# Kernel optimization log

Hardware: AMD Instinct MI355X
Metric: run time of the kernel (lower is better)

## Reference

```python
import math
import jax, jax.numpy as jnp
import numpy as np

D_MODEL = 768
N_HEADS = 12
HEAD_DIM = D_MODEL // N_HEADS
D_FF = 3072
LN_EPS = 1e-5


def _alibi_slopes(n_heads):
    def pow2(n):
        start = 2 ** (-(2 ** (-(math.log2(n) - 3))))
        return [start * start ** i for i in range(n)]
    if n_heads & (n_heads - 1) == 0:
        s = pow2(n_heads)
    else:
        c = 2 ** math.floor(math.log2(n_heads))
        s = pow2(c) + pow2(2 * c)[0::2][: n_heads - c]
    return np.asarray(s, dtype=np.float32)  # positive; negated at use site


def _ln(t, g, b):
    m = jnp.mean(t, axis=-1, keepdims=True)
    v = jnp.mean(jnp.square(t - m), axis=-1, keepdims=True)
    return (t - m) * jax.lax.rsqrt(v + LN_EPS) * g + b


def setup_inputs() -> dict:
    key = jax.random.key(0)
    ks = jax.random.split(key, 12)
    B, N = 4, 1025
    s = 0.02
    inp = {
        "x": jax.random.normal(ks[0], (B, N, D_MODEL), dtype=jnp.float32),
        "positions": jax.random.normal(ks[1], (B, N, 2), dtype=jnp.float32) * 8.0,
        "patch_sizes": jax.random.uniform(ks[2], (B,), dtype=jnp.float32, minval=0.5, maxval=2.0),
        "num_registers": 0,
        "ln1_g": jnp.ones((D_MODEL,), jnp.float32),
        "ln1_b": jnp.zeros((D_MODEL,), jnp.float32),
        "wq": jax.random.normal(ks[3], (D_MODEL, D_MODEL), jnp.float32) * s,
        "bq": jnp.zeros((D_MODEL,), jnp.float32),
        "wk": jax.random.normal(ks[4], (D_MODEL, D_MODEL), jnp.float32) * s,
        "bk": jnp.zeros((D_MODEL,), jnp.float32),
        "wv": jax.random.normal(ks[5], (D_MODEL, D_MODEL), jnp.float32) * s,
        "bv": jnp.zeros((D_MODEL,), jnp.float32),
        "wo": jax.random.normal(ks[6], (D_MODEL, D_MODEL), jnp.float32) * s,
        "bo": jnp.zeros((D_MODEL,), jnp.float32),
        "qn_g": jnp.ones((HEAD_DIM,), jnp.float32),
        "qn_b": jnp.zeros((HEAD_DIM,), jnp.float32),
        "kn_g": jnp.ones((HEAD_DIM,), jnp.float32),
        "kn_b": jnp.zeros((HEAD_DIM,), jnp.float32),
        "ln2_g": jnp.ones((D_MODEL,), jnp.float32),
        "ln2_b": jnp.zeros((D_MODEL,), jnp.float32),
        "w1": jax.random.normal(ks[7], (D_MODEL, D_FF), jnp.float32) * s,
        "b1": jnp.zeros((D_FF,), jnp.float32),
        "w2": jax.random.normal(ks[8], (D_FF, D_MODEL), jnp.float32) * s,
        "b2": jnp.zeros((D_MODEL,), jnp.float32),
    }
    return inp


def reference(x, positions, patch_sizes, num_registers,
              ln1_g, ln1_b, wq, bq, wk, bk, wv, bv, wo, bo,
              qn_g, qn_b, kn_g, kn_b, ln2_g, ln2_b, w1, b1, w2, b2):
    B, N, d = x.shape
    H, HD = N_HEADS, HEAD_DIM

    xn = _ln(x, ln1_g, ln1_b)
    q = (xn @ wq + bq).reshape(B, N, H, HD).transpose(0, 2, 1, 3)  # [B,H,N,HD]
    k = (xn @ wk + bk).reshape(B, N, H, HD).transpose(0, 2, 1, 3)
    v = (xn @ wv + bv).reshape(B, N, H, HD).transpose(0, 2, 1, 3)
    q = _ln(q, qn_g, qn_b)  # qk-norm over head_dim
    k = _ln(k, kn_g, kn_b)

    # 2-D ALiBi bias: [B,H,N,N]
    slopes = jnp.asarray(_alibi_slopes(H))  # positive
    ps = jnp.clip(patch_sizes, 1e-6)[:, None, None]
    diff = positions[:, :, None, :] - positions[:, None, :, :]  # [B,N,N,2]
    dist = jnp.sqrt(jnp.sum(jnp.square(diff), axis=-1)) / ps  # [B,N,N]
    bias = -slopes[None, :, None, None] * dist[:, None, :, :]
    idx = jnp.arange(N)
    special = (idx == 0) | ((idx >= 1) & (idx < 1 + num_registers))  # CLS + registers
    keep = (~special).astype(x.dtype)
    bias = bias * keep[None, None, :, None] * keep[None, None, None, :]

    scale = 1.0 / math.sqrt(HD)
    scores = jnp.einsum('bhqd,bhkd->bhqk', q, k) * scale + bias
    attn = jax.nn.softmax(scores, axis=-1)
    o = jnp.einsum('bhqk,bhkd->bhqd', attn, v)
    o = o.transpose(0, 2, 1, 3).reshape(B, N, d) @ wo + bo
    x = x + o

    xn2 = _ln(x, ln2_g, ln2_b)
    mlp = jax.nn.gelu(xn2 @ w1 + b1, approximate=False) @ w2 + b2
    return x + mlp
```

## Files before the change

kernel.cpp:

```cpp
#include <hip/hip_runtime.h>
#include <hip/hip_bf16.h>
#include <math.h>

typedef __attribute__((ext_vector_type(4))) float f32x4;
typedef __attribute__((ext_vector_type(8))) short short8;

#define DMODEL 768
#define NH 12
#define HD 64
#define DFF 3072
#define KVB 64
#define NSPLIT 3
#define QH 2
#define NP 1040

struct FalseC { static constexpr bool v = false; };
struct TrueC  { static constexpr bool v = true;  };

__device__ __forceinline__ short f2bf(float f) {
    union { float f; unsigned int u; } c; c.f = f;
    unsigned int r = c.u + 0x7FFFu + ((c.u >> 16) & 1u);
    return (short)(r >> 16);
}

__device__ __forceinline__ float bf2f(short s) {
    union { unsigned int u; float f; } c; c.u = ((unsigned int)(unsigned short)s) << 16;
    return c.f;
}

__device__ __forceinline__ void gload16(const void* g, void* l) {
    __builtin_amdgcn_global_load_lds((const __attribute__((address_space(1))) void*)g,
                                     (__attribute__((address_space(3))) void*)l, 16, 0, 0);
}

__device__ __forceinline__ int xcd_swz(int o, int nwg) {
    int q = nwg >> 3, r = nwg & 7, x = o & 7, i = o >> 3;
    return (x < r ? x * (q + 1) : r * (q + 1) + (x - r) * q) + i;
}

__global__ __launch_bounds__(256) void transpose_cast(const float* __restrict__ src,
                                                      short* __restrict__ dst, int K, int Nn) {
    __shared__ float tile[32][33];
    const int n0 = blockIdx.x * 32, k0 = blockIdx.y * 32;
    const int tx = threadIdx.x & 31, ty = threadIdx.x >> 5;
    #pragma unroll
    for (int i = ty; i < 32; i += 8) {
        int k = k0 + i, n = n0 + tx;
        tile[i][tx] = (k < K && n < Nn) ? src[(size_t)k * Nn + n] : 0.f;
    }
    __syncthreads();
    #pragma unroll
    for (int i = ty; i < 32; i += 8) {
        int n = n0 + i, k = k0 + tx;
        if (n < Nn && k < K) dst[(size_t)n * K + k] = f2bf(tile[tx][i]);
    }
}

__global__ void concat_bias(const float* __restrict__ bq, const float* __restrict__ bk,
                            const float* __restrict__ bv, float* __restrict__ out) {
    int i = blockIdx.x * 256 + threadIdx.x;
    if (i < 2304) out[i] = (i < 768) ? bq[i] : (i < 1536 ? bk[i - 768] : bv[i - 1536]);
}

__global__ __launch_bounds__(256) void ln_rows(const float* __restrict__ x, const float* __restrict__ g,
                                               const float* __restrict__ bb, short* __restrict__ out, int M) {
    __shared__ float red[8];
    const int row = blockIdx.x;
    const int tid = threadIdx.x;
    const float* xr = x + (size_t)row * DMODEL;
    float v[3];
    #pragma unroll
    for (int j = 0; j < 3; j++) v[j] = xr[tid + j * 256];
    float s = v[0] + v[1] + v[2];
    #pragma unroll
    for (int mk = 32; mk; mk >>= 1) s += __shfl_xor(s, mk);
    if ((tid & 63) == 0) red[tid >> 6] = s;
    __syncthreads();
    const float mean = (red[0] + red[1] + red[2] + red[3]) * (1.0f / 768.0f);
    float sq = 0.f;
    #pragma unroll
    for (int j = 0; j < 3; j++) { float d = v[j] - mean; sq += d * d; }
    #pragma unroll
    for (int mk = 32; mk; mk >>= 1) sq += __shfl_xor(sq, mk);
    if ((tid & 63) == 0) red[4 + (tid >> 6)] = sq;
    __syncthreads();
    const float var = (red[4] + red[5] + red[6] + red[7]) * (1.0f / 768.0f);
    const float rstd = rsqrtf(var + 1e-5f);
    short* orow = out + (size_t)row * DMODEL;
    #pragma unroll
    for (int j = 0; j < 3; j++) {
        int col = tid + j * 256;
        orow[col] = f2bf((v[j] - mean) * rstd * g[col] + bb[col]);
    }
}

__global__ __launch_bounds__(256) void gemm_qkv(const short* __restrict__ A, const short* __restrict__ Bt,
        const float* __restrict__ bias,
        const float* __restrict__ qg, const float* __restrict__ qb2,
        const float* __restrict__ kg, const float* __restrict__ kb2,
        short* __restrict__ Qb, short* __restrict__ Kb, short* __restrict__ Vtp,
        int M, int B, int Nseq) {
    __shared__ short As[64 * 64];
    __shared__ short Bs[128 * 64];
    const int nbx = 18, nby = (M + 63) / 64;
    const int sid = xcd_swz(blockIdx.x, nbx * nby);
    const int n0 = (sid % nbx) * 128, m0 = (sid / nbx) * 64;
    const int tid = threadIdx.x, w = tid >> 6, lane = tid & 63, g = lane >> 4, cl = lane & 15;
    const int wm = w >> 1, wn = w & 1;
    f32x4 acc[2][4];
    #pragma unroll
    for (int a = 0; a < 2; a++)
        #pragma unroll
        for (int b2 = 0; b2 < 4; b2++) acc[a][b2] = (f32x4){0.f, 0.f, 0.f, 0.f};
    for (int kk = 0; kk < 768; kk += 64) {
        #pragma unroll
        for (int c = 0; c < 1536; c += 256) {
            int ci = c + tid;
            if (ci < 512) {
                int row = ci >> 3, p = ci & 7;
                int arow = m0 + row; if (arow >= M) arow = M - 1;
                gload16(A + (size_t)arow * 768 + kk + ((p ^ (row & 7)) << 3), &As[ci * 8]);
            } else {
                int c2 = ci - 512;
                int row = c2 >> 3, p = c2 & 7;
                gload16(Bt + (size_t)(n0 + row) * 768 + kk + ((p ^ (row & 7)) << 3), &Bs[c2 * 8]);
            }
        }
        __syncthreads();
        #pragma unroll
        for (int kh = 0; kh < 2; ++kh) {
            short8 af[2], bf[4];
            #pragma unroll
            for (int mi = 0; mi < 2; mi++) {
                int ra = wm * 32 + mi * 16 + cl;
                af[mi] = *(const short8*)&As[ra * 64 + ((((kh << 2) + g) ^ (ra & 7)) << 3)];
            }
            #pragma unroll
            for (int ni = 0; ni < 4; ni++) {
                int rb = wn * 64 + ni * 16 + cl;
                bf[ni] = *(const short8*)&Bs[rb * 64 + ((((kh << 2) + g) ^ (rb & 7)) << 3)];
            }
            #pragma unroll
            for (int mi = 0; mi < 2; mi++)
                #pragma unroll
                for (int ni = 0; ni < 4; ni++)
                    acc[mi][ni] = __builtin_amdgcn_mfma_f32_16x16x32_bf16(af[mi], bf[ni], acc[mi][ni], 0, 0, 0);
        }
        __syncthreads();
    }
    const int t = n0 / 768;
    const int h = (n0 - t * 768) / 64 + wn;
    const int b0 = m0 / Nseq, bnd = (b0 + 1) * Nseq;
    float bi[4];
    #pragma unroll
    for (int ni = 0; ni < 4; ni++) bi[ni] = bias[n0 + wn * 64 + ni * 16 + cl];
    if (t < 2) {
        const float* gp = (t == 0) ? qg : kg;
        const float* bp = (t == 0) ? qb2 : kb2;
        float gv[4], bv[4];
        #pragma unroll
        for (int ni = 0; ni < 4; ni++) { gv[ni] = gp[ni * 16 + cl]; bv[ni] = bp[ni * 16 + cl]; }
        short* out = (t == 0) ? Qb : Kb;
        #pragma unroll
        for (int mi = 0; mi < 2; mi++)
            #pragma unroll
            for (int r = 0; r < 4; r++) {
                int row = m0 + wm * 32 + mi * 16 + 4 * g + r;
                float v0 = acc[mi][0][r] + bi[0];
                float v1 = acc[mi][1][r] + bi[1];
                float v2 = acc[mi][2][r] + bi[2];
                float v3 = acc[mi][3][r] + bi[3];
                float sx = v0 + v1 + v2 + v3;
                float sxx = v0 * v0 + v1 * v1 + v2 * v2 + v3 * v3;
                #pragma unroll
                for (int mk = 8; mk; mk >>= 1) { sx += __shfl_xor(sx, mk); sxx += __shfl_xor(sxx, mk); }
                float mean = sx * (1.0f / 64.0f);
                float var = sxx * (1.0f / 64.0f) - mean * mean;
                float rstd = rsqrtf(var + 1e-5f);
                if (row < M) {
                    int bb = (row >= bnd) ? b0 + 1 : b0;
                    int n = row - bb * Nseq;
                    size_t base = (((size_t)bb * NH + h) * Nseq + n) * HD + cl;
                    out[base + 0]  = f2bf(fmaf((v0 - mean) * rstd, gv[0], bv[0]));
                    out[base + 16] = f2bf(fmaf((v1 - mean) * rstd, gv[1], bv[1]));
                    out[base + 32] = f2bf(fmaf((v2 - mean) * rstd, gv[2], bv[2]));
                    out[base + 48] = f2bf(fmaf((v3 - mean) * rstd, gv[3], bv[3]));
                }
            }
    } else {
        #pragma unroll
        for (int mi = 0; mi < 2; mi++)
            #pragma unroll
            for (int r = 0; r < 4; r++) {
                int row = m0 + wm * 32 + mi * 16 + 4 * g + r;
                if (row < M) {
                    int bb = (row >= bnd) ? b0 + 1 : b0;
                    int n = row - bb * Nseq;
                    size_t vb2 = ((size_t)bb * NH + h) * HD + cl;
                    #pragma unroll
                    for (int ni = 0; ni < 4; ni++)
                        Vtp[(vb2 + ni * 16) * NP + n] = f2bf(acc[mi][ni][r] + bi[ni]);
                }
            }
    }
}

template<int EPI, int BM, int BN>
__global__ __launch_bounds__(256) void gemm_bt(const short* __restrict__ A, const short* __restrict__ Bt,
        const float* __restrict__ bias, const float* __restrict__ res, void* __restrict__ Cv,
        int M, int Nn, int K) {
    constexpr int RM = BM / 32, RN = BN / 32;
    __shared__ short As[BM * 64];
    __shared__ short Bs[BN * 64];
    const int nbx = Nn / BN, nby = (M + BM - 1) / BM;
    const int sid = xcd_swz(blockIdx.x, nbx * nby);
    const int n0 = (sid % nbx) * BN, m0 = (sid / nbx) * BM;
    const int tid = threadIdx.x, w = tid >> 6, lane = tid & 63, g = lane >> 4, cl = lane & 15;
    const int wm = w >> 1, wn = w & 1;
    f32x4 acc[RM][RN];
    #pragma unroll
    for (int a = 0; a < RM; a++)
        #pragma unroll
        for (int b2 = 0; b2 < RN; b2++) acc[a][b2] = (f32x4){0.f, 0.f, 0.f, 0.f};
    constexpr int CHA = BM * 8, CHT = (BM + BN) * 8;
    for (int kk = 0; kk < K; kk += 64) {
        #pragma unroll
        for (int c = 0; c < CHT; c += 256) {
            int ci = c + tid;
            if (ci < CHA) {
                int row = ci >> 3, p = ci & 7;
                int arow = m0 + row; if (arow >= M) arow = M - 1;
                gload16(A + (size_t)arow * K + kk + ((p ^ (row & 7)) << 3), &As[ci * 8]);
            } else {
                int c2 = ci - CHA;
                int row = c2 >> 3, p = c2 & 7;
                gload16(Bt + (size_t)(n0 + row) * K + kk + ((p ^ (row & 7)) << 3), &Bs[c2 * 8]);
            }
        }
        __syncthreads();
        #pragma unroll
        for (int kh = 0; kh < 2; ++kh) {
            short8 af[RM], bf[RN];
            #pragma unroll
            for (int mi = 0; mi < RM; mi++) {
                int ra = wm * (BM / 2) + mi * 16 + cl;
                af[mi] = *(const short8*)&As[ra * 64 + ((((kh << 2) + g) ^ (ra & 7)) << 3)];
            }
            #pragma unroll
            for (int ni = 0; ni < RN; ni++) {
                int rb = wn * (BN / 2) + ni * 16 + cl;
                bf[ni] = *(const short8*)&Bs[rb * 64 + ((((kh << 2) + g) ^ (rb & 7)) << 3)];
            }
            #pragma unroll
            for (int mi = 0; mi < RM; mi++)
                #pragma unroll
                for (int ni = 0; ni < RN; ni++)
                    acc[mi][ni] = __builtin_amdgcn_mfma_f32_16x16x32_bf16(af[mi], bf[ni], acc[mi][ni], 0, 0, 0);
        }
        __syncthreads();
    }
    #pragma unroll
    for (int ni = 0; ni < RN; ++ni) {
        int col = n0 + wn * (BN / 2) + ni * 16 + cl;
        float bi = bias[col];
        #pragma unroll
        for (int mi = 0; mi < RM; ++mi) {
            int rb = m0 + wm * (BM / 2) + mi * 16 + 4 * g;
            #pragma unroll
            for (int r = 0; r < 4; ++r) {
                int row = rb + r;
                if (row < M) {
                    float vv = acc[mi][ni][r] + bi;
                    if (EPI == 1) {
                        vv += res[(size_t)row * Nn + col];
                        ((float*)Cv)[(size_t)row * Nn + col] = vv;
                    } else {
                        float ge = 0.5f * vv * (1.0f + erff(vv * 0.70710678118654752f));
                        ((short*)Cv)[(size_t)row * Nn + col] = f2bf(ge);
                    }
                }
            }
        }
    }
}

__global__ __launch_bounds__(256, 3) void attn_kernel(
        const short* __restrict__ Qb, const short* __restrict__ Kb, const short* __restrict__ Vt,
        const float* __restrict__ pos, const float* __restrict__ psz, const int* __restrict__ nregp,
        short* __restrict__ opart, float* __restrict__ ppart, int B, int Nn, int nwg) {
    __shared__ short Vbuf[2][QH][4096];
    __shared__ short Pl[4][QH][16][68];
    __shared__ float Rs[4][QH][16];
    const int nqt = (Nn + 63) >> 6;
    const int sid = xcd_swz(blockIdx.x, nwg);
    const int qt = sid % nqt;
    const int rem = sid / nqt;
    const int nyy = (NH / QH) * NSPLIT;
    const int yy = rem % nyy;
    const int b = rem / nyy;
    const int h0 = (yy / NSPLIT) * QH, sp = yy % NSPLIT;
    const int tid = threadIdx.x, w = tid >> 6, lane = tid & 63, g = lane >> 4, cl = lane & 15;
    const int nreg1 = 1 + nregp[0];
    const float inv_ps = 1.0f / fmaxf(psz[b], 1e-6f);
    const float sc2 = 0.125f * 1.4426950408889634f;
    const size_t bq = (size_t)b * Nn;
    const float2* __restrict__ pos2 = (const float2*)pos;
    const int q0 = qt * 64 + w * 16;

    size_t bh[QH], vb[QH];
    short8 qa[QH][2];
    float sP[QH];
    int qr = q0 + cl; if (qr > Nn - 1) qr = Nn - 1;
    const float2 qp = pos2[bq + qr];
    const float keepq = (qr < nreg1) ? 0.f : 1.f;
    #pragma unroll
    for (int hh = 0; hh < QH; hh++) {
        int h = h0 + hh;
        bh[hh] = ((size_t)b * NH + h) * (size_t)Nn;
        vb[hh] = ((size_t)b * NH + h) * (size_t)(HD * NP);
        float slope = (h < 8) ? exp2f(-(float)(h + 1)) : exp2f(-0.5f - (float)(h - 8));
        sP[hh] = slope * inv_ps * 1.4426950408889634f * keepq;
        const short* qptr = Qb + (bh[hh] + qr) * HD;
        qa[hh][0] = *(const short8*)(qptr + 8 * g);
        qa[hh][1] = *(const short8*)(qptr + 32 + 8 * g);
    }

    int qi[4];
    #pragma unroll
    for (int i = 0; i < 4; i++) qi[i] = q0 + 4 * g + i;

    f32x4 o[QH][4];
    float psum[QH] = {0.f, 0.f};
    #pragma unroll
    for (int hh = 0; hh < QH; hh++)
        #pragma unroll
        for (int c2 = 0; c2 < 4; c2++) o[hh][c2] = (f32x4){0.f, 0.f, 0.f, 0.f};

    const int ktiles = (Nn + KVB - 1) / KVB;
    const int tps = (ktiles + NSPLIT - 1) / NSPLIT;
    const int t0 = sp * tps, t1 = min(ktiles, t0 + tps);

    auto stage = [&](int buf, int kt) {
        const int kv0 = kt * KVB;
        #pragma unroll
        for (int it = 0; it < 2 * QH; ++it) {
            int idx = it * 256 + tid;
            int hh = idx >> 9, rm = idx & 511;
            int d = rm >> 3, slot = rm & 7;
            int kvs = kv0 + ((slot ^ (d & 7)) << 3);
            gload16(Vt + vb[hh] + (size_t)d * NP + kvs, &Vbuf[buf][hh][rm * 8]);
        }
    };

    stage(0, t0);
    int cur = 0;
    for (int kt = t0; kt < t1; ++kt) {
        const int kv0 = kt * KVB;
        __syncthreads();
        if (kt + 1 < t1) stage(cur ^ 1, kt + 1);

        auto qbody = [&](int qt2, auto mc, auto tc) {
            constexpr bool KMASK = decltype(mc)::v;
            constexpr bool TAIL  = decltype(tc)::v;
            const int kbase = kv0 + qt2 * 16;
            int krow = kbase + cl;
            if (TAIL) krow = min(krow, Nn - 1);
            const short* kp0 = Kb + (bh[0] + krow) * HD;
            const short* kp1 = Kb + (bh[1] + krow) * HD;
            const short8 k00 = *(const short8*)(kp0 + 8 * g);
            const short8 k01 = *(const short8*)(kp0 + 32 + 8 * g);
            const short8 k10 = *(const short8*)(kp1 + 8 * g);
            const short8 k11 = *(const short8*)(kp1 + 32 + 8 * g);
            f32x4 s0 = __builtin_amdgcn_mfma_f32_16x16x32_bf16(k00, qa[0][0], (f32x4){0.f,0.f,0.f,0.f}, 0, 0, 0);
            s0 = __builtin_amdgcn_mfma_f32_16x16x32_bf16(k01, qa[0][1], s0, 0, 0, 0);
            f32x4 s1 = __builtin_amdgcn_mfma_f32_16x16x32_bf16(k10, qa[1][0], (f32x4){0.f,0.f,0.f,0.f}, 0, 0, 0);
            s1 = __builtin_amdgcn_mfma_f32_16x16x32_bf16(k11, qa[1][1], s1, 0, 0, 0);
            const int kb4 = kbase + 4 * g;
            float p0v[4], p1v[4];
            #pragma unroll
            for (int i = 0; i < 4; i++) {
                int ki = kb4 + i;
                int kic = TAIL ? min(ki, Nn - 1) : ki;
                float2 kp2 = pos2[bq + kic];
                float dx = qp.x - kp2.x, dy = qp.y - kp2.y;
                float dist = sqrtf(fmaf(dx, dx, dy * dy));
                if (KMASK) dist *= (ki < nreg1) ? 0.f : 1.f;
                float e0 = fmaf(s0[i], sc2, -12.0f);
                e0 = fmaf(-sP[0], dist, e0);
                float p0 = exp2f(e0);
                float e1 = fmaf(s1[i], sc2, -12.0f);
                e1 = fmaf(-sP[1], dist, e1);
                float p1 = exp2f(e1);
                if (TAIL) { bool vl = ki < Nn; p0 = vl ? p0 : 0.f; p1 = vl ? p1 : 0.f; }
                psum[0] += p0; psum[1] += p1;
                p0v[i] = p0; p1v[i] = p1;
            }
            unsigned int w00, w01, w10, w11;
            asm("v_cvt_pk_bf16_f32 %0, %1, %2" : "=v"(w00) : "v"(p0v[0]), "v"(p0v[1]));
            asm("v_cvt_pk_bf16_f32 %0, %1, %2" : "=v"(w01) : "v"(p0v[2]), "v"(p0v[3]));
            asm("v_cvt_pk_bf16_f32 %0, %1, %2" : "=v"(w10) : "v"(p1v[0]), "v"(p1v[1]));
            asm("v_cvt_pk_bf16_f32 %0, %1, %2" : "=v"(w11) : "v"(p1v[2]), "v"(p1v[3]));
            *(unsigned int*)&Pl[w][0][cl][qt2 * 16 + 4 * g]     = w00;
            *(unsigned int*)&Pl[w][0][cl][qt2 * 16 + 4 * g + 2] = w01;
            *(unsigned int*)&Pl[w][1][cl][qt2 * 16 + 4 * g]     = w10;
            *(unsigned int*)&Pl[w][1][cl][qt2 * 16 + 4 * g + 2] = w11;
        };

        const bool istail = (kv0 + KVB > Nn);
        if (!istail) {
            if (kv0 < nreg1) {
                qbody(0, TrueC{}, FalseC{}); qbody(1, TrueC{}, FalseC{});
                qbody(2, TrueC{}, FalseC{}); qbody(3, TrueC{}, FalseC{});
            } else {
                qbody(0, FalseC{}, FalseC{}); qbody(1, FalseC{}, FalseC{});
                qbody(2, FalseC{}, FalseC{}); qbody(3, FalseC{}, FalseC{});
            }
        } else {
            qbody(0, FalseC{}, TrueC{}); qbody(1, FalseC{}, TrueC{});
            qbody(2, FalseC{}, TrueC{}); qbody(3, FalseC{}, TrueC{});
        }

        #pragma unroll
        for (int hh = 0; hh < QH; hh++) {
            #pragma unroll
            for (int ks = 0; ks < 2; ++ks) {
                const short8 pf = *(const short8*)&Pl[w][hh][cl][ks * 32 + 8 * g];
                #pragma unroll
                for (int c2 = 0; c2 < 4; c2++) {
                    const int d = c2 * 16 + cl;
                    const int slot = ((ks << 2) + g) ^ (cl & 7);
                    const short8 vf = *(const short8*)&Vbuf[cur][hh][d * 64 + slot * 8];
                    o[hh][c2] = __builtin_amdgcn_mfma_f32_16x16x32_bf16(pf, vf, o[hh][c2], 0, 0, 0);
                }
            }
        }
        cur ^= 1;
    }

    #pragma unroll
    for (int hh = 0; hh < QH; hh++) {
        float r = psum[hh];
        r += __shfl_xor(r, 16);
        r += __shfl_xor(r, 32);
        if (lane < 16) Rs[w][hh][lane] = r;
    }
    float4 rs0 = *(const float4*)&Rs[w][0][4 * g];
    float4 rs1 = *(const float4*)&Rs[w][1][4 * g];
    #pragma unroll
    for (int i = 0; i < 4; i++) {
        if (qi[i] < Nn) {
            #pragma unroll
            for (int hh = 0; hh < QH; hh++) {
                size_t rbase = (((size_t)sp * B + b) * NH + (h0 + hh)) * Nn + qi[i];
                #pragma unroll
                for (int c2 = 0; c2 < 4; c2++)
                    opart[rbase * HD + c2 * 16 + cl] = f2bf(o[hh][c2][i]);
                if (cl == 0) ppart[rbase] = hh ? rs1[i] : rs0[i];
            }
        }
    }
}

__global__ __launch_bounds__(256) void attn_reduce(const short* __restrict__ opart,
        const float* __restrict__ ppart, short* __restrict__ Ob, int B, int Nn) {
    const int rows = B * NH * Nn;
    const int row = blockIdx.x * 4 + (threadIdx.x >> 6);
    if (row >= rows) return;
    const int d = threadIdx.x & 63;
    const int n = row % Nn;
    const int bh = row / Nn;
    const int h = bh % NH, b = bh / NH;
    const size_t stride = (size_t)B * NH * Nn;
    float o = 0.f, p = 0.f;
    #pragma unroll
    for (int s = 0; s < NSPLIT; s++) {
        o += bf2f(opart[((size_t)s * stride + row) * HD + d]);
        p += ppart[(size_t)s * stride + row];
    }
    Ob[((size_t)b * Nn + n) * DMODEL + h * HD + d] = f2bf(o / p);
}

extern "C" void kernel_launch(void* const* d_in, const int* in_sizes, int n_in,
                              void* d_out, int out_size, void* d_ws, size_t ws_size,
                              hipStream_t stream) {
    const float* x    = (const float*)d_in[0];
    const float* pos  = (const float*)d_in[1];
    const float* psz  = (const float*)d_in[2];
    const int*   nreg = (const int*)d_in[3];
    const float* ln1g = (const float*)d_in[4];
    const float* ln1b = (const float*)d_in[5];
    const float* wq   = (const float*)d_in[6];
    const float* bq   = (const float*)d_in[7];
    const float* wk   = (const float*)d_in[8];
    const float* bk   = (const float*)d_in[9];
    const float* wv   = (const float*)d_in[10];
    const float* bv   = (const float*)d_in[11];
    const float* wo   = (const float*)d_in[12];
    const float* bo   = (const float*)d_in[13];
    const float* qng  = (const float*)d_in[14];
    const float* qnb  = (const float*)d_in[15];
    const float* kng  = (const float*)d_in[16];
    const float* knb  = (const float*)d_in[17];
    const float* ln2g = (const float*)d_in[18];
    const float* ln2b = (const float*)d_in[19];
    const float* w1   = (const float*)d_in[20];
    const float* b1   = (const float*)d_in[21];
    const float* w2   = (const float*)d_in[22];
    const float* b2   = (const float*)d_in[23];

    const int B  = in_sizes[2];
    const int Nn = in_sizes[1] / (2 * B);
    const int M  = B * Nn;

    char* ws = (char*)d_ws;
    size_t off = 0;
    auto alloc = [&](size_t bytes) -> char* {
        char* p = ws + off;
        off += (bytes + 255) & ~(size_t)255;
        return p;
    };
    short* wt_qkv   = (short*)alloc((size_t)2304 * 768 * 2);
    short* wt_o     = (short*)alloc((size_t)768 * 768 * 2);
    short* wt_1     = (short*)alloc((size_t)3072 * 768 * 2);
    short* wt_2     = (short*)alloc((size_t)768 * 3072 * 2);
    float* bias_qkv = (float*)alloc(2304 * 4);
    short* xn       = (short*)alloc((size_t)M * 768 * 2);
    short* Qb       = (short*)alloc((size_t)M * 768 * 2);
    short* Kb       = (short*)alloc((size_t)M * 768 * 2);
    short* Vt       = (short*)alloc((size_t)B * NH * HD * NP * 2 + 4096);
    short* Ob       = (short*)alloc((size_t)M * 768 * 2);
    float* x1       = (float*)alloc((size_t)M * 768 * 4);
    short* xn2      = (short*)alloc((size_t)M * 768 * 2);
    short* hmid     = (short*)alloc((size_t)M * 3072 * 2);
    float* ppart    = (float*)alloc((size_t)NSPLIT * B * NH * Nn * 4);
    short* opart    = hmid;

    dim3 blk(256);
    transpose_cast<<<dim3(24, 24), blk, 0, stream>>>(wq, wt_qkv, 768, 768);
    transpose_cast<<<dim3(24, 24), blk, 0, stream>>>(wk, wt_qkv + 768 * 768, 768, 768);
    transpose_cast<<<dim3(24, 24), blk, 0, stream>>>(wv, wt_qkv + 2 * 768 * 768, 768, 768);
    transpose_cast<<<dim3(24, 24), blk, 0, stream>>>(wo, wt_o, 768, 768);
    transpose_cast<<<dim3(96, 24), blk, 0, stream>>>(w1, wt_1, 768, 3072);
    transpose_cast<<<dim3(24, 96), blk, 0, stream>>>(w2, wt_2, 3072, 768);
    concat_bias<<<9, blk, 0, stream>>>(bq, bk, bv, bias_qkv);

    const int MB64 = (M + 63) / 64;
    const int MB128 = (M + 127) / 128;
    ln_rows<<<M, blk, 0, stream>>>(x, ln1g, ln1b, xn, M);
    gemm_qkv<<<18 * MB64, blk, 0, stream>>>(xn, wt_qkv, bias_qkv, qng, qnb, kng, knb,
                                            Qb, Kb, Vt, M, B, Nn);
    const int nqt = (Nn + 63) / 64;
    const int anwg = nqt * (NH / QH) * NSPLIT * B;
    attn_kernel<<<anwg, blk, 0, stream>>>(Qb, Kb, Vt, pos, psz, nreg, opart, ppart, B, Nn, anwg);
    attn_reduce<<<(B * NH * Nn + 3) / 4, blk, 0, stream>>>(opart, ppart, Ob, B, Nn);
    gemm_bt<1, 64, 64><<<12 * MB64, blk, 0, stream>>>(Ob, wt_o, bo, x, x1, M, 768, 768);
    ln_rows<<<M, blk, 0, stream>>>(x1, ln2g, ln2b, xn2, M);
    gemm_bt<2, 128, 128><<<24 * MB128, blk, 0, stream>>>(xn2, wt_1, b1, nullptr, hmid, M, 3072, 768);
    gemm_bt<1, 64, 64><<<12 * MB64, blk, 0, stream>>>(hmid, wt_2, b2, x1, (float*)d_out, M, 768, 3072);
}
```

Baseline: 283.1 us.

## Merge weight transposes, single-buffer attention V tile, retile FFN1 GEMM

```diff
diff --git a/kernel.cpp b/kernel.cpp
--- a/kernel.cpp
+++ b/kernel.cpp
@@ -38,10 +38,25 @@
     return (x < r ? x * (q + 1) : r * (q + 1) + (x - r) * q) + i;
 }
 
-__global__ __launch_bounds__(256) void transpose_cast(const float* __restrict__ src,
-                                                      short* __restrict__ dst, int K, int Nn) {
+__global__ __launch_bounds__(256) void transpose_all(
+        const float* __restrict__ wq, const float* __restrict__ wk, const float* __restrict__ wv,
+        const float* __restrict__ wo, const float* __restrict__ w1, const float* __restrict__ w2,
+        short* __restrict__ wt_qkv, short* __restrict__ wt_o,
+        short* __restrict__ wt_1, short* __restrict__ wt_2) {
     __shared__ float tile[32][33];
-    const int n0 = blockIdx.x * 32, k0 = blockIdx.y * 32;
+    int bid = blockIdx.x;
+    const float* src; short* dst; int K, Nn, nx;
+    if (bid < 2304) {
+        int s = bid / 576; bid -= s * 576;
+        src = (s == 0) ? wq : (s == 1) ? wk : (s == 2) ? wv : wo;
+        dst = (s < 3) ? (wt_qkv + (size_t)s * 768 * 768) : wt_o;
+        K = 768; Nn = 768; nx = 24;
+    } else if (bid < 4608) {
+        bid -= 2304; src = w1; dst = wt_1; K = 768; Nn = 3072; nx = 96;
+    } else {
+        bid -= 4608; src = w2; dst = wt_2; K = 3072; Nn = 768; nx = 24;
+    }
+    const int n0 = (bid % nx) * 32, k0 = (bid / nx) * 32;
     const int tx = threadIdx.x & 31, ty = threadIdx.x >> 5;
     #pragma unroll
     for (int i = ty; i < 32; i += 8) {
@@ -284,11 +299,11 @@
     }
 }
 
-__global__ __launch_bounds__(256, 3) void attn_kernel(
+__global__ __launch_bounds__(256, 4) void attn_kernel(
         const short* __restrict__ Qb, const short* __restrict__ Kb, const short* __restrict__ Vt,
         const float* __restrict__ pos, const float* __restrict__ psz, const int* __restrict__ nregp,
         short* __restrict__ opart, float* __restrict__ ppart, int B, int Nn, int nwg) {
-    __shared__ short Vbuf[2][QH][4096];
+    __shared__ short Vbuf[QH][4096];
     __shared__ short Pl[4][QH][16][68];
     __shared__ float Rs[4][QH][16];
     const int nqt = (Nn + 63) >> 6;
@@ -340,7 +355,7 @@
     const int tps = (ktiles + NSPLIT - 1) / NSPLIT;
     const int t0 = sp * tps, t1 = min(ktiles, t0 + tps);
 
-    auto stage = [&](int buf, int kt) {
+    auto stage = [&](int kt) {
         const int kv0 = kt * KVB;
         #pragma unroll
         for (int it = 0; it < 2 * QH; ++it) {
@@ -348,16 +363,13 @@
             int hh = idx >> 9, rm = idx & 511;
             int d = rm >> 3, slot = rm & 7;
             int kvs = kv0 + ((slot ^ (d & 7)) << 3);
-            gload16(Vt + vb[hh] + (size_t)d * NP + kvs, &Vbuf[buf][hh][rm * 8]);
+            gload16(Vt + vb[hh] + (size_t)d * NP + kvs, &Vbuf[hh][rm * 8]);
         }
     };
 
-    stage(0, t0);
-    int cur = 0;
+    stage(t0);
     for (int kt = t0; kt < t1; ++kt) {
         const int kv0 = kt * KVB;
-        __syncthreads();
-        if (kt + 1 < t1) stage(cur ^ 1, kt + 1);
 
         auto qbody = [&](int qt2, auto mc, auto tc) {
             constexpr bool KMASK = decltype(mc)::v;
@@ -420,6 +432,8 @@
             qbody(2, FalseC{}, TrueC{}); qbody(3, FalseC{}, TrueC{});
         }
 
+        __syncthreads();
+
         #pragma unroll
         for (int hh = 0; hh < QH; hh++) {
             #pragma unroll
@@ -429,12 +443,14 @@
                 for (int c2 = 0; c2 < 4; c2++) {
                     const int d = c2 * 16 + cl;
                     const int slot = ((ks << 2) + g) ^ (cl & 7);
-                    const short8 vf = *(const short8*)&Vbuf[cur][hh][d * 64 + slot * 8];
+                    const short8 vf = *(const short8*)&Vbuf[hh][d * 64 + slot * 8];
                     o[hh][c2] = __builtin_amdgcn_mfma_f32_16x16x32_bf16(pf, vf, o[hh][c2], 0, 0, 0);
                 }
             }
         }
-        cur ^= 1;
+
+        __syncthreads();
+        if (kt + 1 < t1) stage(kt + 1);
     }
 
     #pragma unroll
@@ -536,16 +552,10 @@
     short* opart    = hmid;
 
     dim3 blk(256);
-    transpose_cast<<<dim3(24, 24), blk, 0, stream>>>(wq, wt_qkv, 768, 768);
-    transpose_cast<<<dim3(24, 24), blk, 0, stream>>>(wk, wt_qkv + 768 * 768, 768, 768);
-    transpose_cast<<<dim3(24, 24), blk, 0, stream>>>(wv, wt_qkv + 2 * 768 * 768, 768, 768);
-    transpose_cast<<<dim3(24, 24), blk, 0, stream>>>(wo, wt_o, 768, 768);
-    transpose_cast<<<dim3(96, 24), blk, 0, stream>>>(w1, wt_1, 768, 3072);
-    transpose_cast<<<dim3(24, 96), blk, 0, stream>>>(w2, wt_2, 3072, 768);
+    transpose_all<<<6912, blk, 0, stream>>>(wq, wk, wv, wo, w1, w2, wt_qkv, wt_o, wt_1, wt_2);
     concat_bias<<<9, blk, 0, stream>>>(bq, bk, bv, bias_qkv);
 
     const int MB64 = (M + 63) / 64;
-    const int MB128 = (M + 127) / 128;
     ln_rows<<<M, blk, 0, stream>>>(x, ln1g, ln1b, xn, M);
     gemm_qkv<<<18 * MB64, blk, 0, stream>>>(xn, wt_qkv, bias_qkv, qng, qnb, kng, knb,
                                             Qb, Kb, Vt, M, B, Nn);
@@ -555,6 +565,6 @@
     attn_reduce<<<(B * NH * Nn + 3) / 4, blk, 0, stream>>>(opart, ppart, Ob, B, Nn);
     gemm_bt<1, 64, 64><<<12 * MB64, blk, 0, stream>>>(Ob, wt_o, bo, x, x1, M, 768, 768);
     ln_rows<<<M, blk, 0, stream>>>(x1, ln2g, ln2b, xn2, M);
-    gemm_bt<2, 128, 128><<<24 * MB128, blk, 0, stream>>>(xn2, wt_1, b1, nullptr, hmid, M, 3072, 768);
+    gemm_bt<2, 64, 128><<<24 * MB64, blk, 0, stream>>>(xn2, wt_1, b1, nullptr, hmid, M, 3072, 768);
     gemm_bt<1, 64, 64><<<12 * MB64, blk, 0, stream>>>(hmid, wt_2, b2, x1, (float*)d_out, M, 768, 3072);
 }
```

After: 258.9 us. 8.5% less time.
